# Optimization experiments

Measured on AMD Instinct MI355X. Metric: run time of the kernel, lower is better.

The kernel has to match this reference:

```python
import math
import jax, jax.numpy as jnp
import numpy as np

GRID = 16          # img_size // patch_size = 224 // 14
N_PER_H = 2048     # n_neurons // n_head = 8192 // 4
THETA = 10000.0


def _freqs_2d():
    """2D RoPE phase table, shape (1, 1, GRID*GRID, N_PER_H).
    Layout per position: [h_phases | w_phases | h_phases | w_phases], each half_dim//2 wide.
    """
    dim = N_PER_H
    half = dim // 2
    inv_freq = 1.0 / THETA ** (jnp.arange(0, half, 2, dtype=jnp.float32) / half)  # (half//2,)
    pos = jnp.arange(GRID, dtype=jnp.float32)
    ph = pos[:, None] * inv_freq[None, :]                       # (GRID, half//2)
    ph_h = jnp.broadcast_to(ph[:, None, :], (GRID, GRID, half // 2))
    ph_w = jnp.broadcast_to(ph[None, :, :], (GRID, GRID, half // 2))
    phases = jnp.concatenate([ph_h, ph_w, ph_h, ph_w], axis=-1)  # (GRID, GRID, dim)
    return phases.reshape(1, 1, GRID * GRID, dim)


def _rope(phases, v):
    ang = (phases % 1.0) * (2.0 * math.pi)
    c = jnp.cos(ang)
    s = jnp.sin(ang)
    # interleaved rotation: (-v_odd, v_even) re-interleaved
    v_rot = jnp.stack((-v[..., 1::2], v[..., ::2]), axis=-1).reshape(v.shape)
    return (v * c).astype(v.dtype) + (v_rot * s).astype(v.dtype)


def setup_inputs() -> dict:
    key = jax.random.key(0)
    kq, kk, kv = jax.random.split(key, 3)
    B, H, T, N = 16, 4, 256, N_PER_H
    D = 256
    Q = jax.random.normal(kq, (B, H, T, N), dtype=jnp.float32)
    K = jax.random.normal(kk, (B, H, T, N), dtype=jnp.float32)
    V = jax.random.normal(kv, (B, 1, T, D), dtype=jnp.float32)
    return {"Q": Q, "K": K, "V": V}


def reference(Q, K, V):
    B, H, T, N = Q.shape
    n_patches = GRID * GRID
    freqs = _freqs_2d()[:, :, :n_patches, :N]
    if T == n_patches + 1:  # static-shape branch (CLS token)
        Qr = jnp.concatenate([Q[:, :, :1, :], _rope(freqs, Q[:, :, 1:, :])], axis=2)
        Kr = jnp.concatenate([K[:, :, :1, :], _rope(freqs, K[:, :, 1:, :])], axis=2)
    else:
        f = freqs[:, :, :T, :]
        Qr = _rope(f, Q)
        Kr = _rope(f, K)
    # non-softmax bidirectional attention
    scores = jnp.einsum('bhtn,bhsn->bhts', Qr, Kr) / math.sqrt(N)  # (B,H,T,T)
    return jnp.matmul(scores, V)  # V (B,1,T,D) broadcasts over H -> (B,H,T,D)
```

## Files before the change

kernel.cpp:

```cpp
#include <hip/hip_runtime.h>
#include <hip/hip_bf16.h>

#define T_  256
#define NN_ 2048

typedef short bf16x8 __attribute__((ext_vector_type(8)));
typedef float f32x4  __attribute__((ext_vector_type(4)));

__device__ __forceinline__ unsigned short f2bf(float x) {
    union { float f; unsigned u; } v; v.f = x;
    unsigned r = v.u + 0x7fffu + ((v.u >> 16) & 1u);
    return (unsigned short)(r >> 16);
}
__device__ __forceinline__ float bflo(unsigned w) {
    union { unsigned u; float f; } v; v.u = w << 16; return v.f;
}
__device__ __forceinline__ float bfhi(unsigned w) {
    union { unsigned u; float f; } v; v.u = w & 0xffff0000u; return v.f;
}
__device__ __forceinline__ unsigned pkbf(float lo, float hi) {
    union { __hip_bfloat16 h; unsigned short s; } a, b;
    a.h = __float2bfloat16(lo);
    b.h = __float2bfloat16(hi);
    return (unsigned)a.s | ((unsigned)b.s << 16);
}

__global__ void build_cs(unsigned* __restrict__ cs) {
    int idx = blockIdx.x * 256 + threadIdx.x;
    int p = idx >> 9, f = idx & 511;
    float inv = powf(10000.0f, -(float)f * (1.0f / 512.0f));
    float ph  = (float)p * inv;
    float ang = (ph - floorf(ph)) * 6.28318530717958647692f;
    float s, c;
    sincosf(ang, &s, &c);
    cs[idx] = pkbf(c, s);
}

__global__ void vtrans(const float* __restrict__ V, unsigned short* __restrict__ Vt) {
    __shared__ unsigned short Tl[64 * 72];
    const int tid = threadIdx.x;
    const int b  = blockIdx.x >> 4;
    const int s0 = ((blockIdx.x >> 2) & 3) << 6;
    const int d0 = (blockIdx.x & 3) << 6;
    const float* Vb = V + (size_t)b * 65536;
#pragma unroll
    for (int u = 0; u < 4; u++) {
        int lin = u * 256 + tid;
        int srow = lin >> 4, c4 = (lin & 15) << 2;
        float4 v = *(const float4*)(Vb + (size_t)(s0 + srow) * 256 + d0 + c4);
        Tl[(c4 + 0) * 72 + srow] = f2bf(v.x);
        Tl[(c4 + 1) * 72 + srow] = f2bf(v.y);
        Tl[(c4 + 2) * 72 + srow] = f2bf(v.z);
        Tl[(c4 + 3) * 72 + srow] = f2bf(v.w);
    }
    __syncthreads();
    unsigned short* Vtb = Vt + (size_t)b * 65536;
#pragma unroll
    for (int u = 0; u < 2; u++) {
        int lin = u * 256 + tid;
        int drow = lin >> 3, sc8 = (lin & 7) << 3;
        *(uint4*)(Vtb + (size_t)(d0 + drow) * 256 + s0 + sc8) =
            *(const uint4*)(&Tl[drow * 72 + sc8]);
    }
}

struct QKSet { float4 a[4]; float4 b[2]; };

__launch_bounds__(512, 4)
__global__ void gemm1(const float* __restrict__ Q, const float* __restrict__ K,
                      const unsigned* __restrict__ cs, unsigned short* __restrict__ scores) {
    __shared__ __align__(16) unsigned short Als[2][128 * 72];
    __shared__ __align__(16) unsigned short Bls[2][64 * 72];
    __shared__ __align__(16) unsigned csl[2][1024];

    const int tid  = threadIdx.x;
    const int bh   = blockIdx.x & 63;
    const int tile = blockIdx.x >> 6;
    const int ti = (tile >> 2) << 7;
    const int si = (tile & 3) << 6;

    const float* Qb = Q + (size_t)bh * (T_ * NN_);
    const float* Kb = K + (size_t)bh * (T_ * NN_);

    const float* qpA[2]; int phA[2], pwA[2], c8A[2], ldsA[2];
    const float* qpB0;   int phB, pwB, c8B, ldsB0;
#pragma unroll
    for (int u = 0; u < 2; u++) {
        int lin = u * 512 + tid;
        int row = lin >> 3, c8 = (lin & 7) << 3;
        int gr = ti + row;
        qpA[u] = Qb + (size_t)gr * NN_ + c8;
        phA[u] = gr >> 4;  pwA[u] = gr & 15;
        c8A[u] = c8;       ldsA[u] = row * 72 + c8;
    }
    {
        int row = tid >> 3, c8 = (tid & 7) << 3;
        int gr = si + row;
        qpB0 = Kb + (size_t)gr * NN_ + c8;
        phB = gr >> 4;  pwB = gr & 15;
        c8B = c8;       ldsB0 = row * 72 + c8;
    }

    const int csE = tid * 2;
    const int csP = csE >> 6, csC = csE & 63;

    const int wv = tid >> 6, lane = tid & 63;
    const int lr = lane & 15, lg = lane >> 4;
    const int m0 = (wv >> 1) << 5;
    const int n0 = (wv & 1) << 5;

    f32x4 acc[2][2];
#pragma unroll
    for (int i = 0; i < 2; i++)
#pragma unroll
        for (int j = 0; j < 2; j++) acc[i][j] = (f32x4){0.f, 0.f, 0.f, 0.f};

    auto LOAD = [&](QKSet& s, int slab) {
        const int k0 = slab << 6;
#pragma unroll
        for (int u = 0; u < 2; u++) {
            s.a[2*u]   = *(const float4*)(qpA[u] + k0);
            s.a[2*u+1] = *(const float4*)(qpA[u] + k0 + 4);
        }
        s.b[0] = *(const float4*)(qpB0 + k0);
        s.b[1] = *(const float4*)(qpB0 + k0 + 4);
    };

    auto CSLOADG = [&](uint2& cr, int slab) {
        const int fk = (slab << 6) & 511;
        cr = *(const uint2*)(cs + (csP << 9) + fk + csC);
    };
    auto CSWRITE = [&](int par, const uint2& cr) {
        *(uint2*)(&csl[par][csE]) = cr;
    };
    auto CSSTD = [&](int par, int slab) {
        const int fk = (slab << 6) & 511;
        *(uint2*)(&csl[par][csE]) = *(const uint2*)(cs + (csP << 9) + fk + csC);
    };

    auto ROT = [&](const float4& f0, const float4& f1,
                   const uint4& u0, const uint4& u1) -> uint4 {
        uint4 o;
        o.x = pkbf(f0.x*bflo(u0.x) - f0.y*bfhi(u0.x),
                   f0.y*bflo(u0.y) + f0.x*bfhi(u0.y));
        o.y = pkbf(f0.z*bflo(u0.z) - f0.w*bfhi(u0.z),
                   f0.w*bflo(u0.w) + f0.z*bfhi(u0.w));
        o.z = pkbf(f1.x*bflo(u1.x) - f1.y*bfhi(u1.x),
                   f1.y*bflo(u1.y) + f1.x*bfhi(u1.y));
        o.w = pkbf(f1.z*bflo(u1.z) - f1.w*bfhi(u1.z),
                   f1.w*bflo(u1.w) + f1.z*bfhi(u1.w));
        return o;
    };

    auto WRITE = [&](int buf, int par, const QKSet& s, int slab) {
        const int w = (slab >> 3) & 1;
#pragma unroll
        for (int u = 0; u < 2; u++) {
            const unsigned* cp = &csl[par][((w ? pwA[u] : phA[u]) << 6) + c8A[u]];
            uint4 u0 = *(const uint4*)cp, u1 = *(const uint4*)(cp + 4);
            *(uint4*)(&Als[buf][ldsA[u]]) = ROT(s.a[2*u], s.a[2*u+1], u0, u1);
        }
        const unsigned* cp = &csl[par][((w ? pwB : phB) << 6) + c8B];
        uint4 u0 = *(const uint4*)cp, u1 = *(const uint4*)(cp + 4);
        *(uint4*)(&Bls[buf][ldsB0]) = ROT(s.b[0], s.b[1], u0, u1);
    };

    auto COMPUTE = [&](int buf) {
        __builtin_amdgcn_s_setprio(1);
#pragma unroll
        for (int kk = 0; kk < 64; kk += 32) {
            bf16x8 af[2], bfr[2];
#pragma unroll
            for (int mi = 0; mi < 2; mi++)
                af[mi] = *(const bf16x8*)(&Als[buf][(m0 + mi * 16 + lr) * 72 + kk + lg * 8]);
#pragma unroll
            for (int ni = 0; ni < 2; ni++)
                bfr[ni] = *(const bf16x8*)(&Bls[buf][(n0 + ni * 16 + lr) * 72 + kk + lg * 8]);
#pragma unroll
            for (int mi = 0; mi < 2; mi++)
#pragma unroll
                for (int ni = 0; ni < 2; ni++)
                    acc[mi][ni] = __builtin_amdgcn_mfma_f32_16x16x32_bf16(
                        af[mi], bfr[ni], acc[mi][ni], 0, 0, 0);
        }
        __builtin_amdgcn_s_setprio(0);
    };

    auto BAR = [&]() {
        asm volatile("s_waitcnt lgkmcnt(0)" ::: "memory");
        __builtin_amdgcn_s_barrier();
        asm volatile("" ::: "memory");
    };

    QKSet s0, s1; uint2 cr0, cr1;

    LOAD(s0, 0);
    LOAD(s1, 1);
    CSSTD(0, 0);
    CSSTD(1, 1);
    CSLOADG(cr0, 2);
    CSLOADG(cr1, 3);
    __builtin_amdgcn_sched_barrier(0);
    BAR();
    WRITE(0, 0, s0, 0);
    LOAD(s0, 2);
    __builtin_amdgcn_sched_barrier(0);
    BAR();

#pragma unroll 1
    for (int t2 = 0; t2 < 15; t2++) {
        const int t = t2 * 2;
        COMPUTE(0);
        WRITE(1, 1, s1, t + 1);
        CSWRITE(0, cr0);
        {
            int s3 = t + 3; if (s3 > 31) s3 = 31;
            int s4 = t + 4; if (s4 > 31) s4 = 31;
            LOAD(s1, s3);
            CSLOADG(cr0, s4);
        }
        __builtin_amdgcn_sched_barrier(0);
        BAR();
        COMPUTE(1);
        WRITE(0, 0, s0, t + 2);
        CSWRITE(1, cr1);
        {
            int s4 = t + 4; if (s4 > 31) s4 = 31;
            int s5 = t + 5; if (s5 > 31) s5 = 31;
            LOAD(s0, s4);
            CSLOADG(cr1, s5);
        }
        __builtin_amdgcn_sched_barrier(0);
        BAR();
    }
    COMPUTE(0);
    WRITE(1, 1, s1, 31);
    BAR();
    COMPUTE(1);

    const float rs = 0.02209708691207961f;
    unsigned short* sb = scores + (size_t)bh * (T_ * T_);
#pragma unroll
    for (int mi = 0; mi < 2; mi++) {
        int tr = ti + m0 + mi * 16 + lg * 4;
#pragma unroll
        for (int ni = 0; ni < 2; ni++) {
            int sc = si + n0 + ni * 16 + lr;
#pragma unroll
            for (int r = 0; r < 4; r++)
                sb[(size_t)(tr + r) * 256 + sc] = f2bf(acc[mi][ni][r] * rs);
        }
    }
}

__launch_bounds__(256, 2)
__global__ void gemm2(const unsigned short* __restrict__ scores,
                      const unsigned short* __restrict__ Vt, float* __restrict__ out) {
    __shared__ __align__(16) unsigned short Als[2][128 * 72];
    __shared__ __align__(16) unsigned short Bls[2][64 * 72];

    const int tid  = threadIdx.x;
    const int bh   = blockIdx.x & 63;
    const int b    = bh >> 2;
    const int tile = blockIdx.x >> 6;
    const int ti = (tile >> 2) << 7;
    const int d0 = (tile & 3) << 6;

    const unsigned short* Sb  = scores + (size_t)bh * 65536;
    const unsigned short* Vtb = Vt + (size_t)b * 65536;

    const int wv = tid >> 6, lane = tid & 63;
    const int lr = lane & 15, lg = lane >> 4;
    const int m0 = (wv >> 1) * 64;
    const int n0 = (wv & 1) * 32;

    f32x4 acc[4][2];
#pragma unroll
    for (int i = 0; i < 4; i++)
#pragma unroll
        for (int j = 0; j < 2; j++) acc[i][j] = (f32x4){0.f, 0.f, 0.f, 0.f};

    uint4 sA[4], sB[2];

    auto LOAD = [&](int k0) {
#pragma unroll
        for (int u = 0; u < 4; u++) {
            int lin = u * 256 + tid;
            int row = lin >> 3, c8 = (lin & 7) << 3;
            sA[u] = *(const uint4*)(Sb + (size_t)(ti + row) * 256 + k0 + c8);
        }
#pragma unroll
        for (int u = 0; u < 2; u++) {
            int lin = u * 256 + tid;
            int row = lin >> 3, c8 = (lin & 7) << 3;
            sB[u] = *(const uint4*)(Vtb + (size_t)(d0 + row) * 256 + k0 + c8);
        }
    };

    auto WRITE = [&](int buf) {
#pragma unroll
        for (int u = 0; u < 4; u++) {
            int lin = u * 256 + tid;
            int row = lin >> 3, c8 = (lin & 7) << 3;
            *(uint4*)(&Als[buf][row * 72 + c8]) = sA[u];
        }
#pragma unroll
        for (int u = 0; u < 2; u++) {
            int lin = u * 256 + tid;
            int row = lin >> 3, c8 = (lin & 7) << 3;
            *(uint4*)(&Bls[buf][row * 72 + c8]) = sB[u];
        }
    };

    auto COMPUTE = [&](int buf) {
        __builtin_amdgcn_s_setprio(1);
#pragma unroll
        for (int kk = 0; kk < 64; kk += 32) {
            bf16x8 af[4], bfr[2];
#pragma unroll
            for (int mi = 0; mi < 4; mi++)
                af[mi] = *(const bf16x8*)(&Als[buf][(m0 + mi * 16 + lr) * 72 + kk + lg * 8]);
#pragma unroll
            for (int ni = 0; ni < 2; ni++)
                bfr[ni] = *(const bf16x8*)(&Bls[buf][(n0 + ni * 16 + lr) * 72 + kk + lg * 8]);
#pragma unroll
            for (int mi = 0; mi < 4; mi++)
#pragma unroll
                for (int ni = 0; ni < 2; ni++)
                    acc[mi][ni] = __builtin_amdgcn_mfma_f32_16x16x32_bf16(
                        af[mi], bfr[ni], acc[mi][ni], 0, 0, 0);
        }
        __builtin_amdgcn_s_setprio(0);
    };

    auto BAR = [&]() {
        asm volatile("s_waitcnt lgkmcnt(0)" ::: "memory");
        __builtin_amdgcn_s_barrier();
        asm volatile("" ::: "memory");
    };

    LOAD(0);
    WRITE(0);
    BAR();

    int cur = 0;
#pragma unroll 1
    for (int t = 0; t < 3; t++) {
        LOAD((t + 1) * 64);
        COMPUTE(cur);
        WRITE(cur ^ 1);
        __builtin_amdgcn_sched_barrier(0);
        BAR();
        cur ^= 1;
    }
    COMPUTE(cur);

    float* ob = out + (size_t)bh * 65536;
#pragma unroll
    for (int mi = 0; mi < 4; mi++) {
        int tr = ti + m0 + mi * 16 + lg * 4;
#pragma unroll
        for (int ni = 0; ni < 2; ni++) {
            int dc = d0 + n0 + ni * 16 + lr;
#pragma unroll
            for (int r = 0; r < 4; r++)
                ob[(size_t)(tr + r) * 256 + dc] = acc[mi][ni][r];
        }
    }
}

extern "C" void kernel_launch(void* const* d_in, const int* in_sizes, int n_in,
                              void* d_out, int out_size, void* d_ws, size_t ws_size,
                              hipStream_t stream) {
    const float* Q = (const float*)d_in[0];
    const float* K = (const float*)d_in[1];
    const float* V = (const float*)d_in[2];
    float* out = (float*)d_out;

    unsigned* cs = (unsigned*)d_ws;
    unsigned short* scores = (unsigned short*)((char*)d_ws + 32768);
    unsigned short* Vt = (unsigned short*)((char*)d_ws + 32768 + 8388608);

    build_cs<<<dim3(32), dim3(256), 0, stream>>>(cs);
    vtrans<<<dim3(256), dim3(256), 0, stream>>>(V, Vt);
    gemm1<<<dim3(512), dim3(512), 0, stream>>>(Q, K, cs, scores);
    gemm2<<<dim3(512), dim3(256), 0, stream>>>(scores, Vt, out);
}
```

Baseline: 131.8 us.

## Split RoPE into separate bf16 pre-cast pass and use direct-to-LDS GEMM kernels

Adds a rope_cast kernel that applies the rotary embedding and scaling to Q and K and writes bf16 copies to workspace. New gemm1b and gemm2b kernels load tiles with global_load_lds into XOR-swizzled LDS. The old fused path stays as a fallback when workspace is too small. The aim is to simplify the GEMM inner loop and cut per-tile rotation work, at the cost of an extra round-trip of 64 MB of bf16 intermediates and a single-buffered loop.

```diff
diff --git a/kernel.cpp b/kernel.cpp
--- a/kernel.cpp
+++ b/kernel.cpp
@@ -23,6 +23,12 @@
     a.h = __float2bfloat16(lo);
     b.h = __float2bfloat16(hi);
     return (unsigned)a.s | ((unsigned)b.s << 16);
+}
+
+__device__ __forceinline__ void gld_lds16(const unsigned short* g, unsigned short* l) {
+    __builtin_amdgcn_global_load_lds(
+        (const __attribute__((address_space(1))) unsigned int*)g,
+        (__attribute__((address_space(3))) unsigned int*)l, 16, 0, 0);
 }
 
 __global__ void build_cs(unsigned* __restrict__ cs) {
@@ -64,6 +70,229 @@
     }
 }
 
+
+__launch_bounds__(256)
+__global__ void rope_cast(const float* __restrict__ Q, const float* __restrict__ K,
+                          const unsigned* __restrict__ cs,
+                          unsigned short* __restrict__ Qr, unsigned short* __restrict__ Kr) {
+    const size_t base = (size_t)blockIdx.x * 256 + threadIdx.x;
+#pragma unroll
+    for (int j = 0; j < 8; j++) {
+        size_t o = base + (size_t)j * 1048576;
+        const float* src;
+        unsigned short* dst;
+        float sc;
+        if (j < 4) { src = Q; dst = Qr; sc = 0.02209708691207961f; }
+        else       { src = K; dst = Kr; sc = 1.0f; o -= 4194304; }
+        const int t = (int)((o >> 8) & 255);
+        const int w = (int)((o >> 6) & 1);
+        const int f = ((int)o & 63) << 3;
+        const int p = w ? (t & 15) : (t >> 4);
+        const float* qp = src + o * 8;
+        float4 q0 = *(const float4*)(qp);
+        float4 q1 = *(const float4*)(qp + 4);
+        const unsigned* cp = cs + (p << 9) + f;
+        uint4 u0 = *(const uint4*)(cp);
+        uint4 u1 = *(const uint4*)(cp + 4);
+        q0.x *= sc; q0.y *= sc; q0.z *= sc; q0.w *= sc;
+        q1.x *= sc; q1.y *= sc; q1.z *= sc; q1.w *= sc;
+        uint4 out;
+        out.x = pkbf(q0.x*bflo(u0.x) - q0.y*bfhi(u0.x),
+                     q0.y*bflo(u0.y) + q0.x*bfhi(u0.y));
+        out.y = pkbf(q0.z*bflo(u0.z) - q0.w*bfhi(u0.z),
+                     q0.w*bflo(u0.w) + q0.z*bfhi(u0.w));
+        out.z = pkbf(q1.x*bflo(u1.x) - q1.y*bfhi(u1.x),
+                     q1.y*bflo(u1.y) + q1.x*bfhi(u1.y));
+        out.w = pkbf(q1.z*bflo(u1.z) - q1.w*bfhi(u1.z),
+                     q1.w*bflo(u1.w) + q1.z*bfhi(u1.w));
+        *(uint4*)(dst + o * 8) = out;
+    }
+}
+
+__launch_bounds__(256)
+__global__ void gemm1b(const unsigned short* __restrict__ Qr,
+                       const unsigned short* __restrict__ Kr,
+                       unsigned short* __restrict__ scores) {
+    __shared__ __align__(16) unsigned short A[128 * 64];
+    __shared__ __align__(16) unsigned short Bt[64 * 64];
+
+    const int tid  = threadIdx.x;
+    const int bh   = blockIdx.x & 63;
+    const int tile = blockIdx.x >> 6;
+    const int ti = (tile >> 2) << 7;
+    const int si = (tile & 3) << 6;
+
+    const unsigned short* Qb = Qr + (size_t)bh * (T_ * NN_);
+    const unsigned short* Kb = Kr + (size_t)bh * (T_ * NN_);
+
+    const unsigned short* srcA[4]; unsigned short* dstA[4];
+    const unsigned short* srcB[2]; unsigned short* dstB[2];
+#pragma unroll
+    for (int u = 0; u < 4; u++) {
+        int lin = u * 256 + tid;
+        int row = lin >> 3, cu = lin & 7;
+        int scol = cu ^ (row & 7);
+        srcA[u] = Qb + (size_t)(ti + row) * NN_ + scol * 8;
+        dstA[u] = &A[lin * 8];
+    }
+#pragma unroll
+    for (int u = 0; u < 2; u++) {
+        int lin = u * 256 + tid;
+        int row = lin >> 3, cu = lin & 7;
+        int scol = cu ^ (row & 7);
+        srcB[u] = Kb + (size_t)(si + row) * NN_ + scol * 8;
+        dstB[u] = &Bt[lin * 8];
+    }
+
+    const int wv = tid >> 6, lane = tid & 63;
+    const int lr = lane & 15, lg = lane >> 4;
+    const int m0 = (wv >> 1) * 64;
+    const int n0 = (wv & 1) * 32;
+
+    f32x4 acc[4][2];
+#pragma unroll
+    for (int i = 0; i < 4; i++)
+#pragma unroll
+        for (int j = 0; j < 2; j++) acc[i][j] = (f32x4){0.f, 0.f, 0.f, 0.f};
+
+    for (int k0 = 0; k0 < NN_; k0 += 64) {
+#pragma unroll
+        for (int u = 0; u < 4; u++) gld_lds16(srcA[u] + k0, dstA[u]);
+#pragma unroll
+        for (int u = 0; u < 2; u++) gld_lds16(srcB[u] + k0, dstB[u]);
+        __syncthreads();
+
+#pragma unroll
+        for (int kk = 0; kk < 64; kk += 32) {
+            bf16x8 af[4], bfr[2];
+#pragma unroll
+            for (int mi = 0; mi < 4; mi++) {
+                int row = m0 + mi * 16 + lr;
+                int c   = (kk >> 3) + lg;
+                af[mi] = *(const bf16x8*)(&A[row * 64 + ((c ^ (row & 7)) << 3)]);
+            }
+#pragma unroll
+            for (int ni = 0; ni < 2; ni++) {
+                int row = n0 + ni * 16 + lr;
+                int c   = (kk >> 3) + lg;
+                bfr[ni] = *(const bf16x8*)(&Bt[row * 64 + ((c ^ (row & 7)) << 3)]);
+            }
+#pragma unroll
+            for (int mi = 0; mi < 4; mi++)
+#pragma unroll
+                for (int ni = 0; ni < 2; ni++)
+                    acc[mi][ni] = __builtin_amdgcn_mfma_f32_16x16x32_bf16(
+                        af[mi], bfr[ni], acc[mi][ni], 0, 0, 0);
+        }
+        __syncthreads();
+    }
+
+    unsigned short* sb = scores + (size_t)bh * (T_ * T_);
+#pragma unroll
+    for (int mi = 0; mi < 4; mi++) {
+        int tr = ti + m0 + mi * 16 + lg * 4;
+#pragma unroll
+        for (int ni = 0; ni < 2; ni++) {
+            int sc = si + n0 + ni * 16 + lr;
+#pragma unroll
+            for (int r = 0; r < 4; r++)
+                sb[(size_t)(tr + r) * 256 + sc] = f2bf(acc[mi][ni][r]);
+        }
+    }
+}
+
+__launch_bounds__(256)
+__global__ void gemm2b(const unsigned short* __restrict__ scores,
+                       const unsigned short* __restrict__ Vt, float* __restrict__ out) {
+    __shared__ __align__(16) unsigned short A[128 * 64];
+    __shared__ __align__(16) unsigned short Bt[64 * 64];
+
+    const int tid  = threadIdx.x;
+    const int bh   = blockIdx.x & 63;
+    const int b    = bh >> 2;
+    const int tile = blockIdx.x >> 6;
+    const int ti = (tile >> 2) << 7;
+    const int d0 = (tile & 3) << 6;
+
+    const unsigned short* Sb  = scores + (size_t)bh * 65536;
+    const unsigned short* Vtb = Vt + (size_t)b * 65536;
+
+    const unsigned short* srcA[4]; unsigned short* dstA[4];
+    const unsigned short* srcB[2]; unsigned short* dstB[2];
+#pragma unroll
+    for (int u = 0; u < 4; u++) {
+        int lin = u * 256 + tid;
+        int row = lin >> 3, cu = lin & 7;
+        int scol = cu ^ (row & 7);
+        srcA[u] = Sb + (size_t)(ti + row) * 256 + scol * 8;
+        dstA[u] = &A[lin * 8];
+    }
+#pragma unroll
+    for (int u = 0; u < 2; u++) {
+        int lin = u * 256 + tid;
+        int row = lin >> 3, cu = lin & 7;
+        int scol = cu ^ (row & 7);
+        srcB[u] = Vtb + (size_t)(d0 + row) * 256 + scol * 8;
+        dstB[u] = &Bt[lin * 8];
+    }
+
+    const int wv = tid >> 6, lane = tid & 63;
+    const int lr = lane & 15, lg = lane >> 4;
+    const int m0 = (wv >> 1) * 64;
+    const int n0 = (wv & 1) * 32;
+
+    f32x4 acc[4][2];
+#pragma unroll
+    for (int i = 0; i < 4; i++)
+#pragma unroll
+        for (int j = 0; j < 2; j++) acc[i][j] = (f32x4){0.f, 0.f, 0.f, 0.f};
+
+    for (int k0 = 0; k0 < 256; k0 += 64) {
+#pragma unroll
+        for (int u = 0; u < 4; u++) gld_lds16(srcA[u] + k0, dstA[u]);
+#pragma unroll
+        for (int u = 0; u < 2; u++) gld_lds16(srcB[u] + k0, dstB[u]);
+        __syncthreads();
+
+#pragma unroll
+        for (int kk = 0; kk < 64; kk += 32) {
+            bf16x8 af[4], bfr[2];
+#pragma unroll
+            for (int mi = 0; mi < 4; mi++) {
+                int row = m0 + mi * 16 + lr;
+                int c   = (kk >> 3) + lg;
+                af[mi] = *(const bf16x8*)(&A[row * 64 + ((c ^ (row & 7)) << 3)]);
+            }
+#pragma unroll
+            for (int ni = 0; ni < 2; ni++) {
+                int row = n0 + ni * 16 + lr;
+                int c   = (kk >> 3) + lg;
+                bfr[ni] = *(const bf16x8*)(&Bt[row * 64 + ((c ^ (row & 7)) << 3)]);
+            }
+#pragma unroll
+            for (int mi = 0; mi < 4; mi++)
+#pragma unroll
+                for (int ni = 0; ni < 2; ni++)
+                    acc[mi][ni] = __builtin_amdgcn_mfma_f32_16x16x32_bf16(
+                        af[mi], bfr[ni], acc[mi][ni], 0, 0, 0);
+        }
+        __syncthreads();
+    }
+
+    float* ob = out + (size_t)bh * 65536;
+#pragma unroll
+    for (int mi = 0; mi < 4; mi++) {
+        int tr = ti + m0 + mi * 16 + lg * 4;
+#pragma unroll
+        for (int ni = 0; ni < 2; ni++) {
+            int dc = d0 + n0 + ni * 16 + lr;
+#pragma unroll
+            for (int r = 0; r < 4; r++)
+                ob[(size_t)(tr + r) * 256 + dc] = acc[mi][ni][r];
+        }
+    }
+}
+
 struct QKSet { float4 a[4]; float4 b[2]; };
 
 __launch_bounds__(512, 4)
@@ -125,7 +354,6 @@
         s.b[0] = *(const float4*)(qpB0 + k0);
         s.b[1] = *(const float4*)(qpB0 + k0 + 4);
     };
-
     auto CSLOADG = [&](uint2& cr, int slab) {
         const int fk = (slab << 6) & 511;
         cr = *(const uint2*)(cs + (csP << 9) + fk + csC);
@@ -137,7 +365,6 @@
         const int fk = (slab << 6) & 511;
         *(uint2*)(&csl[par][csE]) = *(const uint2*)(cs + (csP << 9) + fk + csC);
     };
-
     auto ROT = [&](const float4& f0, const float4& f1,
                    const uint4& u0, const uint4& u1) -> uint4 {
         uint4 o;
@@ -151,7 +378,6 @@
                    f1.w*bflo(u1.w) + f1.z*bfhi(u1.w));
         return o;
     };
-
     auto WRITE = [&](int buf, int par, const QKSet& s, int slab) {
         const int w = (slab >> 3) & 1;
 #pragma unroll
@@ -164,7 +390,6 @@
         uint4 u0 = *(const uint4*)cp, u1 = *(const uint4*)(cp + 4);
         *(uint4*)(&Bls[buf][ldsB0]) = ROT(s.b[0], s.b[1], u0, u1);
     };
-
     auto COMPUTE = [&](int buf) {
         __builtin_amdgcn_s_setprio(1);
 #pragma unroll
@@ -185,7 +410,6 @@
         }
         __builtin_amdgcn_s_setprio(0);
     };
-
     auto BAR = [&]() {
         asm volatile("s_waitcnt lgkmcnt(0)" ::: "memory");
         __builtin_amdgcn_s_barrier();
@@ -193,7 +417,6 @@
     };
 
     QKSet s0, s1; uint2 cr0, cr1;
-
     LOAD(s0, 0);
     LOAD(s1, 1);
     CSSTD(0, 0);
@@ -296,7 +519,6 @@
             sB[u] = *(const uint4*)(Vtb + (size_t)(d0 + row) * 256 + k0 + c8);
         }
     };
-
     auto WRITE = [&](int buf) {
 #pragma unroll
         for (int u = 0; u < 4; u++) {
@@ -311,7 +533,6 @@
             *(uint4*)(&Bls[buf][row * 72 + c8]) = sB[u];
         }
     };
-
     auto COMPUTE = [&](int buf) {
         __builtin_amdgcn_s_setprio(1);
 #pragma unroll
@@ -332,7 +553,6 @@
         }
         __builtin_amdgcn_s_setprio(0);
     };
-
     auto BAR = [&]() {
         asm volatile("s_waitcnt lgkmcnt(0)" ::: "memory");
         __builtin_amdgcn_s_barrier();
@@ -380,9 +600,18 @@
     unsigned* cs = (unsigned*)d_ws;
     unsigned short* scores = (unsigned short*)((char*)d_ws + 32768);
     unsigned short* Vt = (unsigned short*)((char*)d_ws + 32768 + 8388608);
+    unsigned short* Qr = (unsigned short*)((char*)d_ws + 16777216);
+    unsigned short* Kr = (unsigned short*)((char*)d_ws + 83886080);
 
     build_cs<<<dim3(32), dim3(256), 0, stream>>>(cs);
     vtrans<<<dim3(256), dim3(256), 0, stream>>>(V, Vt);
-    gemm1<<<dim3(512), dim3(512), 0, stream>>>(Q, K, cs, scores);
-    gemm2<<<dim3(512), dim3(256), 0, stream>>>(scores, Vt, out);
-}
+
+    if (ws_size >= 150994944ULL) {
+        rope_cast<<<dim3(4096), dim3(256), 0, stream>>>(Q, K, cs, Qr, Kr);
+        gemm1b<<<dim3(512), dim3(256), 0, stream>>>(Qr, Kr, scores);
+        gemm2b<<<dim3(512), dim3(256), 0, stream>>>(scores, Vt, out);
+    } else {
+        gemm1<<<dim3(512), dim3(512), 0, stream>>>(Q, K, cs, scores);
+        gemm2<<<dim3(512), dim3(256), 0, stream>>>(scores, Vt, out);
+    }
+}
```

After: 146.2 us. 1.11x slower.
